# Optimization experiments

Measured on AMD Instinct MI355X. Metric: run time of the kernel, lower is better.

Reference implementation:

```python
import jax, jax.numpy as jnp
import numpy as np
import math

HEAD_DIM = 64
HEAD_NUM = 8  # hidden_dim(512) // head_dim(64)
EPS = 1e-8


def modulated_linear(x, s, weight, aff_w, aff_b):
    # x: [B, N, IN], s: [B, S], weight: [OUT, IN], aff_w: [IN, S], aff_b: [IN]
    style = s @ aff_w.T + aff_b                       # [B, IN]
    w = weight[None, :, :] * style[:, None, :]        # [B, OUT, IN]
    demod = jax.lax.rsqrt(jnp.sum(w * w, axis=2) + EPS)  # [B, OUT]
    w = w * demod[:, :, None]
    return jnp.einsum('bni,boi->bno', x, w)           # [B, N, OUT]


def setup_inputs() -> dict:
    key = jax.random.key(0)
    ks = jax.random.split(key, 8)
    B, N, F, S = 8, 1024, 512, 512
    sc = 1.0 / math.sqrt(F)
    return {
        'x': jax.random.normal(ks[0], (B, N, F), dtype=jnp.float32),
        's': jax.random.normal(ks[1], (B, S), dtype=jnp.float32),
        'k_weight': jax.random.normal(ks[2], (F, F), dtype=jnp.float32) * sc,
        'k_aff_w': jax.random.normal(ks[3], (F, S), dtype=jnp.float32) * sc,
        'k_aff_b': jnp.ones((F,), dtype=jnp.float32),
        'o_weight': jax.random.normal(ks[4], (F, F), dtype=jnp.float32) * sc,
        'o_aff_w': jax.random.normal(ks[5], (F, S), dtype=jnp.float32) * sc,
        'o_aff_b': jnp.ones((F,), dtype=jnp.float32),
    }


def reference(x, s, k_weight, k_aff_w, k_aff_b, o_weight, o_aff_w, o_aff_b):
    B, N, _ = x.shape
    # Original code computes q, k, v all via k_mapping (faithful to the bug).
    kqv = modulated_linear(x, s, k_weight, k_aff_w, k_aff_b)  # [B, N, hidden]
    kqv = kqv.reshape(B, N, HEAD_NUM, HEAD_DIM)               # [B, N, H, D]
    q = k = v = kqv
    scale = 1.0 / math.sqrt(HEAD_DIM)
    scores = jnp.einsum('bnhd,bmhd->bhnm', q, k) * scale      # [B, H, N, N]
    attn = jax.nn.softmax(scores, axis=-1)
    out = jnp.einsum('bhnm,bmhd->bnhd', attn, v)              # [B, N, H, D]
    out = out.reshape(B, N, HEAD_NUM * HEAD_DIM)
    return modulated_linear(out, s, o_weight, o_aff_w, o_aff_b)
```

## Files before the change

### kernel.cpp

```cpp
#include <hip/hip_runtime.h>
#include <stdint.h>

using short8  = __attribute__((ext_vector_type(8))) short;
using f32x4   = __attribute__((ext_vector_type(4))) float;
using float4v = __attribute__((ext_vector_type(4))) float;
using u16x4   = __attribute__((ext_vector_type(4))) unsigned short;

__device__ __forceinline__ unsigned short f2b(float f) {
    union { float f; unsigned int i; } v; v.f = f;
    unsigned int i = v.i;
    unsigned int r = (i + 0x7fffu + ((i >> 16) & 1u)) >> 16;
    return (unsigned short)r;
}
__device__ __forceinline__ short8 ld8(const unsigned short* p) {
    return *reinterpret_cast<const short8*>(p);
}
__device__ __forceinline__ void st8(unsigned short* p, short8 v) {
    *reinterpret_cast<short8*>(p) = v;
}
__device__ __forceinline__ f32x4 mfma16(short8 a, short8 b, f32x4 c) {
    return __builtin_amdgcn_mfma_f32_16x16x32_bf16(a, b, c, 0, 0, 0);
}
__device__ __forceinline__ void stC(float* p, float v)          { *p = v; }
__device__ __forceinline__ void stC(unsigned short* p, float v) { *p = f2b(v); }

__device__ __forceinline__ void gl16(const unsigned short* g, unsigned short* l) {
    __builtin_amdgcn_global_load_lds(
        (const __attribute__((address_space(1))) void*)g,
        (__attribute__((address_space(3))) void*)l,
        16, 0, 0);
}

__device__ __forceinline__ unsigned int cvtpk(float lo, float hi) {
    unsigned int r;
    asm("v_cvt_pk_bf16_f32 %0, %1, %2" : "=v"(r) : "v"(lo), "v"(hi));
    return r;
}
__device__ __forceinline__ void pl32swap(unsigned int& a, unsigned int& b) {
    asm("v_permlane32_swap_b32 %0, %1" : "+v"(a), "+v"(b));
}
__device__ __forceinline__ void pl16swap(unsigned int& a, unsigned int& b) {
    asm("v_permlane16_swap_b32 %0, %1" : "+v"(a), "+v"(b));
}
__device__ __forceinline__ short8 pack4(unsigned int x0, unsigned int x1,
                                        unsigned int x2, unsigned int x3) {
    union { unsigned int u[4]; short8 s; } c;
    c.u[0] = x0; c.u[1] = x1; c.u[2] = x2; c.u[3] = x3;
    return c.s;
}

__global__ __launch_bounds__(256) void cvt_kernel(
    const float* __restrict__ x, unsigned short* __restrict__ xb)
{
    int i = (blockIdx.x * 256 + threadIdx.x) * 8;
    float4v v0 = *reinterpret_cast<const float4v*>(x + i);
    float4v v1 = *reinterpret_cast<const float4v*>(x + i + 4);
    short8 o;
#pragma unroll
    for (int j = 0; j < 4; ++j) o[j] = (short)f2b(v0[j]);
#pragma unroll
    for (int j = 0; j < 4; ++j) o[4 + j] = (short)f2b(v1[j]);
    st8(xb + i, o);
}

__global__ __launch_bounds__(256) void style_kernel(
    const float* __restrict__ s,
    const float* __restrict__ k_aff_w, const float* __restrict__ k_aff_b,
    const float* __restrict__ o_aff_w, const float* __restrict__ o_aff_b,
    float* __restrict__ style)
{
    int wid  = blockIdx.x * 4 + (threadIdx.x >> 6);
    int lane = threadIdx.x & 63;
    int map  = wid >> 12;
    int rem  = wid & 4095;
    int b    = rem >> 9;
    int i    = rem & 511;
    const float* aw = map ? o_aff_w : k_aff_w;
    const float* ab = map ? o_aff_b : k_aff_b;
    const float* sp = s  + b * 512 + lane * 8;
    const float* wp = aw + i * 512 + lane * 8;
    float acc = 0.f;
#pragma unroll
    for (int j = 0; j < 8; ++j) acc += sp[j] * wp[j];
#pragma unroll
    for (int off = 1; off < 64; off <<= 1) acc += __shfl_xor(acc, off, 64);
    if (lane == 0) style[(map * 8 + b) * 512 + i] = acc + ab[i];
}

__global__ __launch_bounds__(256) void modw_kernel(
    const float* __restrict__ k_weight,
    const float* __restrict__ o_weight,
    const float* __restrict__ style,
    unsigned short* __restrict__ wmod)
{
    int wid  = blockIdx.x * 4 + (threadIdx.x >> 6);
    int lane = threadIdx.x & 63;
    int map  = wid >> 12;
    int rem  = wid & 4095;
    int b    = rem >> 9;
    int o    = rem & 511;
    const float* wrow = (map ? o_weight : k_weight) + o * 512 + lane * 8;
    const float* st   = style + (map * 8 + b) * 512 + lane * 8;
    float w[8]; float ss = 0.f;
#pragma unroll
    for (int j = 0; j < 8; ++j) { w[j] = wrow[j] * st[j]; ss += w[j] * w[j]; }
#pragma unroll
    for (int off = 1; off < 64; off <<= 1) ss += __shfl_xor(ss, off, 64);
    float demod = rsqrtf(ss + 1e-8f);
    short8 ov;
#pragma unroll
    for (int j = 0; j < 8; ++j) ov[j] = (short)f2b(w[j] * demod);
    unsigned short* dst = wmod + (((size_t)map * 8 + b) * 512 + o) * 512 + lane * 8;
    *reinterpret_cast<short8*>(dst) = ov;
}

template <typename CT, bool WVT>
__global__ __launch_bounds__(256) void gemm_bt_lds_kernel(
    const unsigned short* __restrict__ A,
    const unsigned short* __restrict__ Bt,
    CT* __restrict__ C,
    unsigned short* __restrict__ VT)
{
    __shared__ __align__(16) unsigned short smem[4 * 4096];

    int blk = blockIdx.x;
    int b   = blk & 7;
    int rem = blk >> 3;
    int mt  = rem & 15;
    int nt  = rem >> 4;
    int tid  = threadIdx.x;
    int w    = tid >> 6;
    int lane = tid & 63;
    int quad = lane >> 4;
    int r    = lane & 15;
    int wm   = w >> 1;
    int wn   = w & 1;

    const unsigned short* Ab = A  + ((size_t)b * 1024 + mt * 64) * 512;
    const unsigned short* Bb = Bt + ((size_t)b * 512  + nt * 64) * 512;

    int lrow = lane >> 3;
    int lunit = (lane & 7) ^ lrow;
    int laneoff = lrow * 512 + lunit * 8;

    f32x4 acc[2][2];
#pragma unroll
    for (int i = 0; i < 2; ++i)
#pragma unroll
        for (int j = 0; j < 2; ++j) acc[i][j] = f32x4{0.f, 0.f, 0.f, 0.f};

    auto stage = [&](int sbuf, int kt) {
        int ko = kt * 64;
        unsigned short* Asb = smem + sbuf * 4096;
        unsigned short* Bsb = smem + 8192 + sbuf * 4096;
#pragma unroll
        for (int c = 0; c < 2; ++c) {
            int chunk = w * 2 + c;
            gl16(Ab + (size_t)chunk * 8 * 512 + laneoff + ko, Asb + chunk * 512);
            gl16(Bb + (size_t)chunk * 8 * 512 + laneoff + ko, Bsb + chunk * 512);
        }
    };
    auto frag = [&](int row, int kh) {
        return row * 64 + ((((kh << 2) | quad) ^ (row & 7)) << 3);
    };

    stage(0, 0);
    __syncthreads();

#pragma unroll
    for (int ks = 0; ks < 8; ++ks) {
        int s = ks & 1;
        if (ks < 7) stage(s ^ 1, ks + 1);
        const unsigned short* Ap = smem + s * 4096;
        const unsigned short* Bp = smem + 8192 + s * 4096;
#pragma unroll
        for (int kh = 0; kh < 2; ++kh) {
            short8 af[2], bf[2];
#pragma unroll
            for (int i = 0; i < 2; ++i)
                af[i] = ld8(Ap + frag(wm * 32 + i * 16 + r, kh));
#pragma unroll
            for (int j = 0; j < 2; ++j)
                bf[j] = ld8(Bp + frag(wn * 32 + j * 16 + r, kh));
#pragma unroll
            for (int i = 0; i < 2; ++i)
#pragma unroll
                for (int j = 0; j < 2; ++j)
                    acc[i][j] = mfma16(af[i], bf[j], acc[i][j]);
        }
        __syncthreads();
    }

    CT* Cb = C + (size_t)b * 1024 * 512;
#pragma unroll
    for (int i = 0; i < 2; ++i)
#pragma unroll
        for (int rr = 0; rr < 4; ++rr) {
            int row = mt * 64 + wm * 32 + i * 16 + quad * 4 + rr;
#pragma unroll
            for (int j = 0; j < 2; ++j) {
                int col = nt * 64 + wn * 32 + j * 16 + r;
                stC(Cb + (size_t)row * 512 + col, acc[i][j][rr]);
            }
        }
    if (WVT) {
        constexpr int TP = 72;
        unsigned short (*Tt)[TP] = reinterpret_cast<unsigned short (*)[TP]>(smem);
#pragma unroll
        for (int i = 0; i < 2; ++i)
#pragma unroll
            for (int j = 0; j < 2; ++j) {
                int d = wn * 32 + j * 16 + r;
#pragma unroll
                for (int rh = 0; rh < 2; ++rh) {
                    int tok = wm * 32 + i * 16 + quad * 4 + rh * 2;
                    unsigned int pv = (unsigned int)f2b(acc[i][j][rh * 2]) |
                                      ((unsigned int)f2b(acc[i][j][rh * 2 + 1]) << 16);
                    *reinterpret_cast<unsigned int*>(&Tt[d][tok]) = pv;
                }
            }
        __syncthreads();
        int d  = tid >> 2;
        int cc = tid & 3;
        const unsigned short* src = &Tt[d][cc * 16];
        unsigned short* dst = VT + ((size_t)(b * 8 + nt) * 64 + d) * 1024 + mt * 64 + cc * 16;
        short8 t0 = ld8(src), t1 = ld8(src + 8);
        st8(dst,     t0);
        st8(dst + 8, t1);
    }
}

__global__ __launch_bounds__(256) void attn_kernel(
    const unsigned short* __restrict__ kqv,
    const unsigned short* __restrict__ vt,
    unsigned short* __restrict__ attn_out)
{
    int blk = blockIdx.x;
    int bh = blk & 63;
    int qt = blk >> 6;
    int b  = bh >> 3, h = bh & 7;
    int tid  = threadIdx.x;
    int lane = tid & 63;
    int quad = lane >> 4;
    int r    = lane & 15;

    const unsigned short* Mb = kqv + (size_t)b * 1024 * 512;
    int wv = tid >> 6;
    int q0 = qt * 128 + wv * 32;

    const unsigned short* qpA = Mb + (size_t)(q0 + r) * 512 + h * 64 + quad * 8;
    const unsigned short* qpB = Mb + (size_t)(q0 + 16 + r) * 512 + h * 64 + quad * 8;
    short8 aq0 = ld8(qpA), aq1 = ld8(qpA + 32);
    short8 cq0 = ld8(qpB), cq1 = ld8(qpB + 32);

    short8 ones;
#pragma unroll
    for (int j = 0; j < 8; ++j) ones[j] = (short)0x3F80;

    f32x4 z = {0.f, 0.f, 0.f, 0.f};
    f32x4 oA0 = z, oA1 = z, oA2 = z, oA3 = z, lA = z;
    f32x4 oB0 = z, oB1 = z, oB2 = z, oB3 = z, lB = z;

    const unsigned short* Kg = Mb + h * 64;
    const unsigned short* Vg = vt + (size_t)bh * 64 * 1024;

    const float c  = 0.18033688011112042f;
    const float CM = 28.853900817779268f;

    auto packP = [&](const f32x4* st_, short8& ap0, short8& ap1) {
        unsigned int pk_[4][2];
#pragma unroll
        for (int t = 0; t < 4; ++t)
#pragma unroll
            for (int h2 = 0; h2 < 2; ++h2)
                pk_[t][h2] = cvtpk(exp2f(st_[t][2 * h2]     * c - CM),
                                   exp2f(st_[t][2 * h2 + 1] * c - CM));
        unsigned int a0 = pk_[0][0], b0 = pk_[1][0];
        pl32swap(a0, b0); pl16swap(a0, b0);
        unsigned int a1 = pk_[0][1], b1 = pk_[1][1];
        pl32swap(a1, b1); pl16swap(a1, b1);
        unsigned int c0 = pk_[2][0], d0 = pk_[3][0];
        pl32swap(c0, d0); pl16swap(c0, d0);
        unsigned int c1 = pk_[2][1], d1 = pk_[3][1];
        pl32swap(c1, d1); pl16swap(c1, d1);
        ap0 = pack4(a0, a1, b0, b1);
        ap1 = pack4(c0, c1, d0, d1);
    };

#pragma unroll 2
    for (int it = 0; it < 16; ++it) {
        int k0 = it * 64;
        f32x4 sA[4], sB[4];
#pragma unroll
        for (int t = 0; t < 4; ++t) {
            const unsigned short* kp = Kg + (size_t)(k0 + t * 16 + r) * 512 + quad * 8;
            short8 ka = ld8(kp);
            short8 kb = ld8(kp + 32);
            f32x4 accA = z, accB = z;
            accA = mfma16(ka, aq0, accA);  accA = mfma16(kb, aq1, accA);
            accB = mfma16(ka, cq0, accB);  accB = mfma16(kb, cq1, accB);
            sA[t] = accA;  sB[t] = accB;
        }
        short8 apA0, apA1, apB0, apB1;
        packP(sA, apA0, apA1);
        packP(sB, apB0, apB1);
        {
            const unsigned short* vp0 = Vg + (size_t)(0 * 16 + r) * 1024 + k0 + quad * 8;
            const unsigned short* vp1 = Vg + (size_t)(1 * 16 + r) * 1024 + k0 + quad * 8;
            const unsigned short* vp2 = Vg + (size_t)(2 * 16 + r) * 1024 + k0 + quad * 8;
            const unsigned short* vp3 = Vg + (size_t)(3 * 16 + r) * 1024 + k0 + quad * 8;
            short8 va, vb;
            va = ld8(vp0);  vb = ld8(vp0 + 32);
            oA0 = mfma16(apA0, va, oA0);  oA0 = mfma16(apA1, vb, oA0);
            oB0 = mfma16(apB0, va, oB0);  oB0 = mfma16(apB1, vb, oB0);
            va = ld8(vp1);  vb = ld8(vp1 + 32);
            oA1 = mfma16(apA0, va, oA1);  oA1 = mfma16(apA1, vb, oA1);
            oB1 = mfma16(apB0, va, oB1);  oB1 = mfma16(apB1, vb, oB1);
            va = ld8(vp2);  vb = ld8(vp2 + 32);
            oA2 = mfma16(apA0, va, oA2);  oA2 = mfma16(apA1, vb, oA2);
            oB2 = mfma16(apB0, va, oB2);  oB2 = mfma16(apB1, vb, oB2);
            va = ld8(vp3);  vb = ld8(vp3 + 32);
            oA3 = mfma16(apA0, va, oA3);  oA3 = mfma16(apA1, vb, oA3);
            oB3 = mfma16(apB0, va, oB3);  oB3 = mfma16(apB1, vb, oB3);
            lA = mfma16(apA0, ones, lA);  lA = mfma16(apA1, ones, lA);
            lB = mfma16(apB0, ones, lB);  lB = mfma16(apB1, ones, lB);
        }
    }

    unsigned short* ob = attn_out + (size_t)b * 1024 * 512 + (size_t)h * 64;
#pragma unroll
    for (int rr = 0; rr < 4; ++rr) {
        float invA = 1.0f / lA[rr];
        int nA = q0 + quad * 4 + rr;
        unsigned short* orowA = ob + (size_t)nA * 512 + r;
        orowA[0]  = f2b(oA0[rr] * invA);
        orowA[16] = f2b(oA1[rr] * invA);
        orowA[32] = f2b(oA2[rr] * invA);
        orowA[48] = f2b(oA3[rr] * invA);
        float invB = 1.0f / lB[rr];
        int nB = q0 + 16 + quad * 4 + rr;
        unsigned short* orowB = ob + (size_t)nB * 512 + r;
        orowB[0]  = f2b(oB0[rr] * invB);
        orowB[16] = f2b(oB1[rr] * invB);
        orowB[32] = f2b(oB2[rr] * invB);
        orowB[48] = f2b(oB3[rr] * invB);
    }
}

extern "C" void kernel_launch(void* const* d_in, const int* in_sizes, int n_in,
                              void* d_out, int out_size, void* d_ws, size_t ws_size,
                              hipStream_t stream)
{
    const float* x        = (const float*)d_in[0];
    const float* s        = (const float*)d_in[1];
    const float* k_weight = (const float*)d_in[2];
    const float* k_aff_w  = (const float*)d_in[3];
    const float* k_aff_b  = (const float*)d_in[4];
    const float* o_weight = (const float*)d_in[5];
    const float* o_aff_w  = (const float*)d_in[6];
    const float* o_aff_b  = (const float*)d_in[7];
    float* out = (float*)d_out;

    char* ws = (char*)d_ws;
    float* style          = (float*)ws;
    unsigned short* wmod  = (unsigned short*)(ws + 32 * 1024);
    unsigned short* attn  = wmod + (size_t)2 * 8 * 512 * 512;
    unsigned short* kqv   = attn + (size_t)8 * 1024 * 512;
    unsigned short* vt    = kqv  + (size_t)8 * 1024 * 512;
    unsigned short* xb    = vt   + (size_t)64 * 64 * 1024;

    cvt_kernel  <<<2048, 256, 0, stream>>>(x, xb);
    style_kernel<<<2048, 256, 0, stream>>>(s, k_aff_w, k_aff_b, o_aff_w, o_aff_b, style);
    modw_kernel <<<2048, 256, 0, stream>>>(k_weight, o_weight, style, wmod);
    gemm_bt_lds_kernel<unsigned short, true><<<1024, 256, 0, stream>>>(xb, wmod, kqv, vt);
    attn_kernel<<<512, 256, 0, stream>>>(kqv, vt, attn);
    gemm_bt_lds_kernel<float, false><<<1024, 256, 0, stream>>>(attn, wmod + (size_t)8 * 512 * 512, out, nullptr);
}
```

Before: 172.5 us.

## Stage K/V tiles in double-buffered LDS with register prefetch in attention

The attention kernel now loads K and V tiles cooperatively into padded, double-buffered shared memory instead of having each wave read them straight from global memory. Global loads for the next iteration are issued into registers and written to LDS after compute, with one barrier per iteration. The key loop is split into two independent halves with separate accumulators that are summed at the end, which adds instruction-level parallelism. This cuts redundant global traffic across the four waves, at the cost of more registers (a second accumulator set plus the prefetch buffers) and LDS use that may lower occupancy.

```diff
diff --git a/kernel.cpp b/kernel.cpp
--- a/kernel.cpp
+++ b/kernel.cpp
@@ -235,6 +235,7 @@
     const unsigned short* __restrict__ vt,
     unsigned short* __restrict__ attn_out)
 {
+    constexpr int PAD = 72;
     int blk = blockIdx.x;
     int bh = blk & 63;
     int qt = blk >> 6;
@@ -244,6 +245,9 @@
     int quad = lane >> 4;
     int r    = lane & 15;
 
+    __shared__ __align__(16) unsigned short klds[2][2][64][PAD];
+    __shared__ __align__(16) unsigned short vlds[2][2][64][PAD];
+
     const unsigned short* Mb = kqv + (size_t)b * 1024 * 512;
     int wv = tid >> 6;
     int q0 = qt * 128 + wv * 32;
@@ -258,11 +262,26 @@
     for (int j = 0; j < 8; ++j) ones[j] = (short)0x3F80;
 
     f32x4 z = {0.f, 0.f, 0.f, 0.f};
-    f32x4 oA0 = z, oA1 = z, oA2 = z, oA3 = z, lA = z;
-    f32x4 oB0 = z, oB1 = z, oB2 = z, oB3 = z, lB = z;
-
+    f32x4 oXA0 = z, oXA1 = z, oXA2 = z, oXA3 = z, lXA = z;
+    f32x4 oXB0 = z, oXB1 = z, oXB2 = z, oXB3 = z, lXB = z;
+    f32x4 oYA0 = z, oYA1 = z, oYA2 = z, oYA3 = z, lYA = z;
+    f32x4 oYB0 = z, oYB1 = z, oYB2 = z, oYB3 = z, lYB = z;
+
+    int srow0 = tid >> 3;
+    int srow1 = srow0 + 32;
+    int scol  = (tid & 7) * 8;
     const unsigned short* Kg = Mb + h * 64;
     const unsigned short* Vg = vt + (size_t)bh * 64 * 1024;
+
+#pragma unroll
+    for (int hf = 0; hf < 2; ++hf) {
+        int koff = hf * 512;
+        st8(&klds[0][hf][srow0][scol], ld8(Kg + (size_t)(koff + srow0) * 512 + scol));
+        st8(&klds[0][hf][srow1][scol], ld8(Kg + (size_t)(koff + srow1) * 512 + scol));
+        st8(&vlds[0][hf][srow0][scol], ld8(Vg + (size_t)srow0 * 1024 + koff + scol));
+        st8(&vlds[0][hf][srow1][scol], ld8(Vg + (size_t)srow1 * 1024 + koff + scol));
+    }
+    __syncthreads();
 
     const float c  = 0.18033688011112042f;
     const float CM = 28.853900817779268f;
@@ -286,46 +305,88 @@
         ap0 = pack4(a0, a1, b0, b1);
         ap1 = pack4(c0, c1, d0, d1);
     };
-
-#pragma unroll 2
-    for (int it = 0; it < 16; ++it) {
-        int k0 = it * 64;
-        f32x4 sA[4], sB[4];
+    auto qk = [&](const unsigned short (*kl)[PAD], f32x4* sA, f32x4* sB) {
 #pragma unroll
         for (int t = 0; t < 4; ++t) {
-            const unsigned short* kp = Kg + (size_t)(k0 + t * 16 + r) * 512 + quad * 8;
-            short8 ka = ld8(kp);
-            short8 kb = ld8(kp + 32);
+            short8 ka = ld8(&kl[t * 16 + r][quad * 8]);
+            short8 kb = ld8(&kl[t * 16 + r][32 + quad * 8]);
             f32x4 accA = z, accB = z;
             accA = mfma16(ka, aq0, accA);  accA = mfma16(kb, aq1, accA);
             accB = mfma16(ka, cq0, accB);  accB = mfma16(kb, cq1, accB);
             sA[t] = accA;  sB[t] = accB;
         }
-        short8 apA0, apA1, apB0, apB1;
-        packP(sA, apA0, apA1);
-        packP(sB, apB0, apB1);
-        {
-            const unsigned short* vp0 = Vg + (size_t)(0 * 16 + r) * 1024 + k0 + quad * 8;
-            const unsigned short* vp1 = Vg + (size_t)(1 * 16 + r) * 1024 + k0 + quad * 8;
-            const unsigned short* vp2 = Vg + (size_t)(2 * 16 + r) * 1024 + k0 + quad * 8;
-            const unsigned short* vp3 = Vg + (size_t)(3 * 16 + r) * 1024 + k0 + quad * 8;
-            short8 va, vb;
-            va = ld8(vp0);  vb = ld8(vp0 + 32);
-            oA0 = mfma16(apA0, va, oA0);  oA0 = mfma16(apA1, vb, oA0);
-            oB0 = mfma16(apB0, va, oB0);  oB0 = mfma16(apB1, vb, oB0);
-            va = ld8(vp1);  vb = ld8(vp1 + 32);
-            oA1 = mfma16(apA0, va, oA1);  oA1 = mfma16(apA1, vb, oA1);
-            oB1 = mfma16(apB0, va, oB1);  oB1 = mfma16(apB1, vb, oB1);
-            va = ld8(vp2);  vb = ld8(vp2 + 32);
-            oA2 = mfma16(apA0, va, oA2);  oA2 = mfma16(apA1, vb, oA2);
-            oB2 = mfma16(apB0, va, oB2);  oB2 = mfma16(apB1, vb, oB2);
-            va = ld8(vp3);  vb = ld8(vp3 + 32);
-            oA3 = mfma16(apA0, va, oA3);  oA3 = mfma16(apA1, vb, oA3);
-            oB3 = mfma16(apB0, va, oB3);  oB3 = mfma16(apB1, vb, oB3);
-            lA = mfma16(apA0, ones, lA);  lA = mfma16(apA1, ones, lA);
-            lB = mfma16(apB0, ones, lB);  lB = mfma16(apB1, ones, lB);
-        }
+    };
+    auto pv = [&](const unsigned short (*vl)[PAD],
+                  short8 apA0, short8 apA1, short8 apB0, short8 apB1,
+                  f32x4& oA0, f32x4& oA1, f32x4& oA2, f32x4& oA3, f32x4& lA,
+                  f32x4& oB0, f32x4& oB1, f32x4& oB2, f32x4& oB3, f32x4& lB) {
+        short8 va, vb;
+        va = ld8(&vl[0 * 16 + r][quad * 8]);
+        vb = ld8(&vl[0 * 16 + r][32 + quad * 8]);
+        oA0 = mfma16(apA0, va, oA0);  oA0 = mfma16(apA1, vb, oA0);
+        oB0 = mfma16(apB0, va, oB0);  oB0 = mfma16(apB1, vb, oB0);
+        va = ld8(&vl[1 * 16 + r][quad * 8]);
+        vb = ld8(&vl[1 * 16 + r][32 + quad * 8]);
+        oA1 = mfma16(apA0, va, oA1);  oA1 = mfma16(apA1, vb, oA1);
+        oB1 = mfma16(apB0, va, oB1);  oB1 = mfma16(apB1, vb, oB1);
+        va = ld8(&vl[2 * 16 + r][quad * 8]);
+        vb = ld8(&vl[2 * 16 + r][32 + quad * 8]);
+        oA2 = mfma16(apA0, va, oA2);  oA2 = mfma16(apA1, vb, oA2);
+        oB2 = mfma16(apB0, va, oB2);  oB2 = mfma16(apB1, vb, oB2);
+        va = ld8(&vl[3 * 16 + r][quad * 8]);
+        vb = ld8(&vl[3 * 16 + r][32 + quad * 8]);
+        oA3 = mfma16(apA0, va, oA3);  oA3 = mfma16(apA1, vb, oA3);
+        oB3 = mfma16(apB0, va, oB3);  oB3 = mfma16(apB1, vb, oB3);
+        lA = mfma16(apA0, ones, lA);  lA = mfma16(apA1, ones, lA);
+        lB = mfma16(apB0, ones, lB);  lB = mfma16(apB1, ones, lB);
+    };
+
+    for (int it = 0; it < 8; ++it) {
+        int s = it & 1;
+        short8 pf[8];
+        if (it < 7) {
+            int k0n = (it + 1) * 64;
+            pf[0] = ld8(Kg + (size_t)(k0n + srow0) * 512 + scol);
+            pf[1] = ld8(Kg + (size_t)(k0n + srow1) * 512 + scol);
+            pf[2] = ld8(Kg + (size_t)(512 + k0n + srow0) * 512 + scol);
+            pf[3] = ld8(Kg + (size_t)(512 + k0n + srow1) * 512 + scol);
+            pf[4] = ld8(Vg + (size_t)srow0 * 1024 + k0n + scol);
+            pf[5] = ld8(Vg + (size_t)srow1 * 1024 + k0n + scol);
+            pf[6] = ld8(Vg + (size_t)srow0 * 1024 + 512 + k0n + scol);
+            pf[7] = ld8(Vg + (size_t)srow1 * 1024 + 512 + k0n + scol);
+        }
+        f32x4 sXA[4], sXB[4];
+        qk(klds[s][0], sXA, sXB);
+        short8 apXA0, apXA1, apXB0, apXB1;
+        packP(sXA, apXA0, apXA1);
+        packP(sXB, apXB0, apXB1);
+        f32x4 sYA[4], sYB[4];
+        qk(klds[s][1], sYA, sYB);
+        short8 apYA0, apYA1, apYB0, apYB1;
+        packP(sYA, apYA0, apYA1);
+        packP(sYB, apYB0, apYB1);
+        pv(vlds[s][0], apXA0, apXA1, apXB0, apXB1,
+           oXA0, oXA1, oXA2, oXA3, lXA, oXB0, oXB1, oXB2, oXB3, lXB);
+        pv(vlds[s][1], apYA0, apYA1, apYB0, apYB1,
+           oYA0, oYA1, oYA2, oYA3, lYA, oYB0, oYB1, oYB2, oYB3, lYB);
+        if (it < 7) {
+            int ns = s ^ 1;
+            st8(&klds[ns][0][srow0][scol], pf[0]);
+            st8(&klds[ns][0][srow1][scol], pf[1]);
+            st8(&klds[ns][1][srow0][scol], pf[2]);
+            st8(&klds[ns][1][srow1][scol], pf[3]);
+            st8(&vlds[ns][0][srow0][scol], pf[4]);
+            st8(&vlds[ns][0][srow1][scol], pf[5]);
+            st8(&vlds[ns][1][srow0][scol], pf[6]);
+            st8(&vlds[ns][1][srow1][scol], pf[7]);
+        }
+        __syncthreads();
     }
+
+    f32x4 oA0 = oXA0 + oYA0, oA1 = oXA1 + oYA1;
+    f32x4 oA2 = oXA2 + oYA2, oA3 = oXA3 + oYA3, lA = lXA + lYA;
+    f32x4 oB0 = oXB0 + oYB0, oB1 = oXB1 + oYB1;
+    f32x4 oB2 = oXB2 + oYB2, oB3 = oXB3 + oYB3, lB = lXB + lYB;
 
     unsigned short* ob = attn_out + (size_t)b * 1024 * 512 + (size_t)h * 64;
 #pragma unroll
```

After: 140.0 us. 18.9% less time.
